# Kernel tuning notes

Hardware: AMD Instinct MI355X
Metric: run time of the kernel (lower is better)

The kernel has to match this reference:

```python
import jax, jax.numpy as jnp
import numpy as np

LN_EPS = 1e-5


def setup_inputs() -> dict:
    key = jax.random.key(0)
    k1, k2, k3, k4, k5 = jax.random.split(key, 5)
    N, D, E, T = 100000, 128, 400000, 4  # nodes, feat dim, edges per etype, n etypes
    feat = jax.random.normal(k1, (N, D), dtype=jnp.float32)
    W = jax.random.normal(k2, (T, D, D), dtype=jnp.float32)
    Wf = jax.random.normal(k3, (T, D, 2 * D), dtype=jnp.float32)
    ln_w = jnp.ones((D,), dtype=jnp.float32)
    ln_b = jnp.zeros((D,), dtype=jnp.float32)
    src = jax.random.randint(k4, (T, E), 0, N, dtype=jnp.int32)
    dst = jax.random.randint(k5, (T, E), 0, N, dtype=jnp.int32)
    return {"feat": feat, "W": W, "Wf": Wf, "ln_w": ln_w, "ln_b": ln_b, "src": src, "dst": dst}


def reference(feat, W, Wf, ln_w, ln_b, src, dst):
    N, D = feat.shape
    T = W.shape[0]
    h = jnp.zeros((N, D), dtype=feat.dtype)
    for t in range(T):  # small fixed loop over edge types (structurally distinct weights)
        msg = feat @ W[t]                    # [N, D] per-src-node projection
        fw = feat @ Wf[t]                    # [N, 2D] FiLM params (dst ntype == src ntype)
        gamma, beta = fw[:, :D], fw[:, D:]
        m = jax.nn.relu(gamma * msg + beta)  # node-wise FiLM + ReLU, pre-scatter
        # copy_u -> gather message at edge src; fn.sum -> segment-sum into dst
        h = h + jax.ops.segment_sum(m[src[t]], dst[t], num_segments=N)
    # LayerNorm (elementwise affine); dropout omitted (eval mode)
    mu = jnp.mean(h, axis=-1, keepdims=True)
    var = jnp.mean(jnp.square(h - mu), axis=-1, keepdims=True)
    out = (h - mu) * jax.lax.rsqrt(var + LN_EPS) * ln_w + ln_b
    return out
```

## Files before the change

### kernel.cpp

```cpp
#include <hip/hip_runtime.h>
#include <hip/hip_bf16.h>

#define DD 128
#define LN_EPS 1e-5f
#define BCAP 3072
#define MAXBIN 1024
#define CHUNK 4096

typedef __bf16 bf16x8 __attribute__((ext_vector_type(8)));
typedef float f32x4 __attribute__((ext_vector_type(4)));

__device__ __forceinline__ float bflo(unsigned int u) { return __uint_as_float(u << 16); }
__device__ __forceinline__ float bfhi(unsigned int u) { return __uint_as_float(u & 0xffff0000u); }

__device__ __forceinline__ void gload_lds16(const void* g, void* lds) {
    __builtin_amdgcn_global_load_lds(
        (const __attribute__((address_space(1))) unsigned int*)g,
        (__attribute__((address_space(3))) unsigned int*)lds, 16, 0, 0);
}

__global__ __launch_bounds__(256) void k_head(const float* __restrict__ feat,
                                              const float* __restrict__ W,
                                              const float* __restrict__ Wf,
                                              const int* __restrict__ dst,
                                              unsigned short* __restrict__ fb,
                                              unsigned short* __restrict__ wcat,
                                              int* __restrict__ H,
                                              int E4, int NBLK, int NBIN, int n8) {
    __shared__ int h[MAXBIN];
    const int b = blockIdx.x, tid = threadIdx.x;

    if (b < NBLK) {
        for (int j = tid; j < NBIN; j += 256) h[j] = 0;
        __syncthreads();
        int base = b * CHUNK;
        int end = base + CHUNK < E4 ? base + CHUNK : E4;
        for (int i = base + tid; i < end; i += 256) atomicAdd(&h[dst[i] >> 7], 1);
        __syncthreads();
        for (int j = tid; j < NBIN; j += 256) H[(size_t)j * NBLK + b] = h[j];
    }

    const int gtid = b * 256 + tid, gsz = gridDim.x * 256;

    for (int i = gtid; i < n8; i += gsz) {
        const float4* p = (const float4*)feat + (size_t)i * 2;
        float4 v0 = p[0], v1 = p[1];
        float vv[8] = {v0.x, v0.y, v0.z, v0.w, v1.x, v1.y, v1.z, v1.w};
        unsigned short u[8];
#pragma unroll
        for (int j = 0; j < 8; j++) {
            __hip_bfloat16 bb = __float2bfloat16(vv[j]);
            u[j] = *reinterpret_cast<unsigned short*>(&bb);
        }
        uint4 o;
        o.x = u[0] | ((unsigned)u[1] << 16);
        o.y = u[2] | ((unsigned)u[3] << 16);
        o.z = u[4] | ((unsigned)u[5] << 16);
        o.w = u[6] | ((unsigned)u[7] << 16);
        ((uint4*)fb)[i] = o;
    }

    for (int i = gtid; i < 4 * 384 * 128; i += gsz) {
        int t = i / (384 * 128);
        int r = i % (384 * 128);
        int c = r / 128, k = r % 128;
        float v = (c < 128) ? W[((size_t)t * 128 + k) * 128 + c]
                            : Wf[((size_t)t * 128 + k) * 256 + (c - 128)];
        __hip_bfloat16 bb = __float2bfloat16(v);
        wcat[i] = *reinterpret_cast<unsigned short*>(&bb);
    }
}

__global__ __launch_bounds__(256) void k_scanbin(int* __restrict__ H, int* __restrict__ C,
                                                 int NBLK, int NBIN) {
    const int wv = (blockIdx.x * 256 + threadIdx.x) >> 6;
    const int lane = threadIdx.x & 63;
    if (wv >= NBIN) return;
    int* row = H + (size_t)wv * NBLK;
    int run = 0;
    for (int base = 0; base < NBLK; base += 64) {
        int idx = base + lane;
        int v = (idx < NBLK) ? row[idx] : 0;
        int s = v;
#pragma unroll
        for (int o = 1; o < 64; o <<= 1) {
            int u = __shfl_up(s, o, 64);
            if (lane >= o) s += u;
        }
        if (idx < NBLK) row[idx] = run + s - v;
        run += __shfl(s, 63, 64);
    }
    if (lane == 0) C[wv] = run;
}

__global__ __launch_bounds__(1024) void k_scan(const int* __restrict__ cnt,
                                               int* __restrict__ off, int NB) {
    __shared__ int s[1024];
    int tid = threadIdx.x;
    s[tid] = (tid < NB) ? cnt[tid] : 0;
    __syncthreads();
    for (int st = 1; st < 1024; st <<= 1) {
        int t = s[tid];
        int a = (tid >= st) ? s[tid - st] : 0;
        __syncthreads();
        s[tid] = t + a;
        __syncthreads();
    }
    if (tid < NB) {
        off[tid] = s[tid] - cnt[tid];
        if (tid == NB - 1) off[NB] = s[tid];
    }
}

__global__ __launch_bounds__(256) void k_place2(const int* __restrict__ src,
                                                const int* __restrict__ dst,
                                                const int* __restrict__ H,
                                                const int* __restrict__ binoff,
                                                unsigned int* __restrict__ rec,
                                                int N, int E, int E4, int NBLK, int NBIN) {
    __shared__ int fill[MAXBIN];
    const int b = blockIdx.x;
    for (int j = threadIdx.x; j < NBIN; j += 256)
        fill[j] = binoff[j] + H[(size_t)j * NBLK + b];
    __syncthreads();
    int base = b * CHUNK;
    int end = base + CHUNK < E4 ? base + CHUNK : E4;
    for (int i = base + threadIdx.x; i < end; i += 256) {
        int d = dst[i];
        int t = i / E;
        unsigned int r = ((unsigned)(d & 127) << 19) | (unsigned)(t * N + src[i]);
        int pos = atomicAdd(&fill[d >> 7], 1);
        rec[pos] = r;
    }
}

__global__ __launch_bounds__(256) void k_sortout(const unsigned int* __restrict__ rec,
                                                 const int* __restrict__ binoff,
                                                 unsigned int* __restrict__ sortedg,
                                                 int* __restrict__ nodestart,
                                                 int* __restrict__ nodedeg, int N) {
    __shared__ int lcnt[128], soff[128], sfill[128], tmp[128];
    __shared__ unsigned int sorted[BCAP];
    const int b = blockIdx.x, tid = threadIdx.x;
    const int s0 = binoff[b];
    int n = binoff[b + 1] - s0;
    if (n > BCAP) n = BCAP;

    if (tid < 128) lcnt[tid] = 0;
    __syncthreads();
    for (int j = tid; j < n; j += 256) atomicAdd(&lcnt[rec[s0 + j] >> 19], 1);
    __syncthreads();
    if (tid < 128) tmp[tid] = lcnt[tid];
    __syncthreads();
    for (int st = 1; st < 128; st <<= 1) {
        int t = 0, a = 0;
        if (tid < 128) {
            t = tmp[tid];
            a = (tid >= st) ? tmp[tid - st] : 0;
        }
        __syncthreads();
        if (tid < 128) tmp[tid] = t + a;
        __syncthreads();
    }
    if (tid < 128) {
        int ex = tmp[tid] - lcnt[tid];
        soff[tid] = ex;
        sfill[tid] = ex;
    }
    __syncthreads();
    for (int j = tid; j < n; j += 256) {
        unsigned int r = rec[s0 + j];
        int p = atomicAdd(&sfill[r >> 19], 1);
        sorted[p] = r & 0x7FFFFu;
    }
    __syncthreads();
    for (int j = tid; j < n; j += 256) sortedg[s0 + j] = sorted[j];
    if (tid < 128) {
        int node = b * 128 + tid;
        if (node < N) {
            nodestart[node] = s0 + soff[tid];
            nodedeg[node] = lcnt[tid];
        }
    }
}

__global__ __launch_bounds__(256, 2) void k_gemm_film(const unsigned short* __restrict__ featb,
                                                      const unsigned short* __restrict__ wcat,
                                                      unsigned short* __restrict__ m, int N,
                                                      int NT) {
    __shared__ unsigned char smem[2 * 16384];
    const int t = blockIdx.y;
    const int tid = threadIdx.x;
    const int w = tid >> 6, lane = tid & 63;
    const int lr = lane & 15, kg = lane >> 4;
    const int cbase = w * 32;

    const unsigned short* wt = wcat + (size_t)t * 384 * 128;
    bf16x8 B[4][3][2];
#pragma unroll
    for (int kkI = 0; kkI < 4; kkI++)
#pragma unroll
        for (int mat = 0; mat < 3; mat++)
#pragma unroll
            for (int cj = 0; cj < 2; cj++) {
                int col = mat * 128 + cbase + cj * 16 + lr;
                B[kkI][mat][cj] = *(const bf16x8*)(wt + (size_t)col * 128 + kkI * 32 + kg * 8);
            }

    auto stage = [&](int buf, int r0) {
#pragma unroll
        for (int it = 0; it < 4; it++) {
            int row = it * 16 + w * 4 + (lane >> 4);
            int gr = r0 + row;
            if (gr >= N) gr = N - 1;
            int x = ((lane & 15) * 16) ^ ((row & 7) << 4);
            const unsigned char* g = (const unsigned char*)featb + (size_t)gr * 256 + x;
            gload_lds16(g, smem + buf * 16384 + it * 4096 + w * 1024);
        }
    };

    unsigned short* mt = m + (size_t)t * N * DD;
    int buf = 0;
    int tile = blockIdx.x;
    if (tile < NT) stage(0, tile * 64);

    for (; tile < NT; tile += gridDim.x) {
        __syncthreads();
        int nxt = tile + gridDim.x;
        if (nxt < NT) stage(buf ^ 1, nxt * 64);

        const unsigned char* sm = smem + buf * 16384;
        f32x4 acc[4][3][2] = {};
#pragma unroll
        for (int kkI = 0; kkI < 4; kkI++) {
            bf16x8 a[4];
#pragma unroll
            for (int mi = 0; mi < 4; mi++) {
                int row = mi * 16 + lr;
                int kb = kkI * 64 + kg * 16;
                a[mi] = *(const bf16x8*)(sm + row * 256 + (kb ^ ((row & 7) << 4)));
            }
#pragma unroll
            for (int mi = 0; mi < 4; mi++)
#pragma unroll
                for (int mat = 0; mat < 3; mat++)
#pragma unroll
                    for (int cj = 0; cj < 2; cj++)
                        acc[mi][mat][cj] = __builtin_amdgcn_mfma_f32_16x16x32_bf16(
                            a[mi], B[kkI][mat][cj], acc[mi][mat][cj], 0, 0, 0);
        }

        const int r0 = tile * 64;
#pragma unroll
        for (int mi = 0; mi < 4; mi++)
#pragma unroll
            for (int cj = 0; cj < 2; cj++)
#pragma unroll
                for (int r = 0; r < 4; r++) {
                    int row = r0 + mi * 16 + kg * 4 + r;
                    if (row < N) {
                        float v = acc[mi][1][cj][r] * acc[mi][0][cj][r] + acc[mi][2][cj][r];
                        v = fmaxf(v, 0.0f);
                        __hip_bfloat16 bb = __float2bfloat16(v);
                        mt[(size_t)row * DD + cbase + cj * 16 + lr] =
                            *reinterpret_cast<unsigned short*>(&bb);
                    }
                }
        buf ^= 1;
    }
}

__global__ __launch_bounds__(256) void k_agg_ln(const unsigned int* __restrict__ sortedg,
                                                const int* __restrict__ nodestart,
                                                const int* __restrict__ nodedeg,
                                                const char* __restrict__ mbase,
                                                const float* __restrict__ lnw,
                                                const float* __restrict__ lnb,
                                                float* __restrict__ out, int N) {
    const int wv = threadIdx.x >> 6, lane = threadIdx.x & 63;
    const int node = blockIdx.x * 4 + wv;
    if (node >= N) return;
    const int start = nodestart[node], deg = nodedeg[node];
    const int q = lane >> 4, sl = lane & 15;
    const unsigned soff = (unsigned)sl * 16u;

    float a[8] = {0.f, 0.f, 0.f, 0.f, 0.f, 0.f, 0.f, 0.f};

    int e = 0;
    for (; e + 16 <= deg; e += 16) {
        unsigned r0 = sortedg[start + e + q];
        unsigned r1 = sortedg[start + e + 4 + q];
        unsigned r2 = sortedg[start + e + 8 + q];
        unsigned r3 = sortedg[start + e + 12 + q];
        uint4 p0 = *(const uint4*)(mbase + (r0 * 256u + soff));
        uint4 p1 = *(const uint4*)(mbase + (r1 * 256u + soff));
        uint4 p2 = *(const uint4*)(mbase + (r2 * 256u + soff));
        uint4 p3 = *(const uint4*)(mbase + (r3 * 256u + soff));
        a[0] += bflo(p0.x) + bflo(p1.x) + bflo(p2.x) + bflo(p3.x);
        a[1] += bfhi(p0.x) + bfhi(p1.x) + bfhi(p2.x) + bfhi(p3.x);
        a[2] += bflo(p0.y) + bflo(p1.y) + bflo(p2.y) + bflo(p3.y);
        a[3] += bfhi(p0.y) + bfhi(p1.y) + bfhi(p2.y) + bfhi(p3.y);
        a[4] += bflo(p0.z) + bflo(p1.z) + bflo(p2.z) + bflo(p3.z);
        a[5] += bfhi(p0.z) + bfhi(p1.z) + bfhi(p2.z) + bfhi(p3.z);
        a[6] += bflo(p0.w) + bflo(p1.w) + bflo(p2.w) + bflo(p3.w);
        a[7] += bfhi(p0.w) + bfhi(p1.w) + bfhi(p2.w) + bfhi(p3.w);
    }
    for (; e + 4 <= deg; e += 4) {
        unsigned r0 = sortedg[start + e + q];
        uint4 p0 = *(const uint4*)(mbase + (r0 * 256u + soff));
        a[0] += bflo(p0.x);
        a[1] += bfhi(p0.x);
        a[2] += bflo(p0.y);
        a[3] += bfhi(p0.y);
        a[4] += bflo(p0.z);
        a[5] += bfhi(p0.z);
        a[6] += bflo(p0.w);
        a[7] += bfhi(p0.w);
    }
    if (e < deg) {
        int idx = e + q;
        float w = (idx < deg) ? 1.0f : 0.0f;
        if (idx >= deg) idx = deg - 1;
        unsigned r0 = sortedg[start + idx];
        uint4 p0 = *(const uint4*)(mbase + (r0 * 256u + soff));
        a[0] += w * bflo(p0.x);
        a[1] += w * bfhi(p0.x);
        a[2] += w * bflo(p0.y);
        a[3] += w * bfhi(p0.y);
        a[4] += w * bflo(p0.z);
        a[5] += w * bfhi(p0.z);
        a[6] += w * bflo(p0.w);
        a[7] += w * bfhi(p0.w);
    }

#pragma unroll
    for (int j = 0; j < 8; j++) {
        a[j] += __shfl_xor(a[j], 16, 64);
        a[j] += __shfl_xor(a[j], 32, 64);
    }
    float s = 0.f, ss = 0.f;
#pragma unroll
    for (int j = 0; j < 8; j++) {
        s += a[j];
        ss += a[j] * a[j];
    }
#pragma unroll
    for (int o = 1; o < 16; o <<= 1) {
        s += __shfl_xor(s, o, 64);
        ss += __shfl_xor(ss, o, 64);
    }
    float mu = s * (1.0f / 128.0f);
    float var = ss * (1.0f / 128.0f) - mu * mu;
    float rstd = rsqrtf(var + LN_EPS);
    if (q == 0) {
        float4 w0 = ((const float4*)lnw)[sl * 2];
        float4 w1 = ((const float4*)lnw)[sl * 2 + 1];
        float4 b0 = ((const float4*)lnb)[sl * 2];
        float4 b1 = ((const float4*)lnb)[sl * 2 + 1];
        float4 o0, o1;
        o0.x = (a[0] - mu) * rstd * w0.x + b0.x;
        o0.y = (a[1] - mu) * rstd * w0.y + b0.y;
        o0.z = (a[2] - mu) * rstd * w0.z + b0.z;
        o0.w = (a[3] - mu) * rstd * w0.w + b0.w;
        o1.x = (a[4] - mu) * rstd * w1.x + b1.x;
        o1.y = (a[5] - mu) * rstd * w1.y + b1.y;
        o1.z = (a[6] - mu) * rstd * w1.z + b1.z;
        o1.w = (a[7] - mu) * rstd * w1.w + b1.w;
        ((float4*)(out + (size_t)node * DD))[sl * 2] = o0;
        ((float4*)(out + (size_t)node * DD))[sl * 2 + 1] = o1;
    }
}

extern "C" void kernel_launch(void* const* d_in, const int* in_sizes, int n_in,
                              void* d_out, int out_size, void* d_ws, size_t ws_size,
                              hipStream_t stream) {
    const float* feat = (const float*)d_in[0];
    const float* W    = (const float*)d_in[1];
    const float* Wf   = (const float*)d_in[2];
    const float* lnw  = (const float*)d_in[3];
    const float* lnb  = (const float*)d_in[4];
    const int* src    = (const int*)d_in[5];
    const int* dst    = (const int*)d_in[6];
    float* out = (float*)d_out;

    const int N = in_sizes[0] / DD;
    const int E = in_sizes[5] / 4;
    const int E4 = 4 * E;
    const int NB = (N + 127) >> 7;
    const int NBLK = (E4 + CHUNK - 1) / CHUNK;
    const int NT = (N + 63) / 64;
    const int n8 = N * DD / 8;

    size_t off = 0;
    char* ws = (char*)d_ws;
    auto alloc = [&](size_t bytes) -> void* {
        void* p = ws + off;
        off += (bytes + 255) & ~(size_t)255;
        return p;
    };
    unsigned short* m     = (unsigned short*)alloc((size_t)4 * N * DD * 2);
    unsigned short* featb = (unsigned short*)alloc((size_t)N * DD * 2);
    unsigned short* wcat  = (unsigned short*)alloc((size_t)4 * 384 * 128 * 2);
    int* H      = (int*)alloc((size_t)NB * NBLK * 4);
    int* C      = (int*)alloc((size_t)NB * 4);
    int* binoff = (int*)alloc((size_t)(NB + 1) * 4);
    unsigned int* rec     = (unsigned int*)alloc((size_t)E4 * 4);
    unsigned int* sortedg = (unsigned int*)alloc((size_t)E4 * 4);
    int* nodestart = (int*)alloc((size_t)N * 4);
    int* nodedeg   = (int*)alloc((size_t)N * 4);
    if (off > ws_size) return;

    k_head<<<2 * NBLK, 256, 0, stream>>>(feat, W, Wf, dst, featb, wcat, H,
                                         E4, NBLK, NB, n8);
    k_scanbin<<<(NB * 64 + 255) / 256, 256, 0, stream>>>(H, C, NBLK, NB);
    k_scan<<<1, 1024, 0, stream>>>(C, binoff, NB);
    k_place2<<<NBLK, 256, 0, stream>>>(src, dst, H, binoff, rec, N, E, E4, NBLK, NB);
    k_sortout<<<NB, 256, 0, stream>>>(rec, binoff, sortedg, nodestart, nodedeg, N);
    dim3 gg(128, 4);
    k_gemm_film<<<gg, 256, 0, stream>>>(featb, wcat, m, N, NT);
    k_agg_ln<<<(N + 3) / 4, 256, 0, stream>>>(sortedg, nodestart, nodedeg,
                                              (const char*)m, lnw, lnb, out, N);
}
```

Measured before the change: 178.0 us.

## Fold bin-offset scan into scanbin via last-block ticket; stage edge indices in LDS

Removes the separate single-block k_scan launch by having the last block of k_scanbin (found with an atomic ticket reset in k_head) compute the global bin offsets. Packs per-node start and degree into one int2 array. In the aggregation kernel, each block cooperatively loads its four nodes' contiguous edge-index range into shared memory before the gather, with a global-memory fallback when it exceeds capacity. This trades a kernel launch and scattered index loads for extra block syncs, a threadfence/atomic handoff, and added shared memory per block.

```diff
diff --git a/kernel.cpp b/kernel.cpp
--- a/kernel.cpp
+++ b/kernel.cpp
@@ -6,6 +6,7 @@
 #define BCAP 3072
 #define MAXBIN 1024
 #define CHUNK 4096
+#define EIDX_CAP 1024
 
 typedef __bf16 bf16x8 __attribute__((ext_vector_type(8)));
 typedef float f32x4 __attribute__((ext_vector_type(4)));
@@ -25,10 +26,11 @@
                                               const int* __restrict__ dst,
                                               unsigned short* __restrict__ fb,
                                               unsigned short* __restrict__ wcat,
-                                              int* __restrict__ H,
+                                              int* __restrict__ H, int* __restrict__ ticket,
                                               int E4, int NBLK, int NBIN, int n8) {
     __shared__ int h[MAXBIN];
     const int b = blockIdx.x, tid = threadIdx.x;
+    if (b == 0 && tid == 0) *ticket = 0;
 
     if (b < NBLK) {
         for (int j = tid; j < NBIN; j += 256) h[j] = 0;
@@ -72,44 +74,68 @@
 }
 
 __global__ __launch_bounds__(256) void k_scanbin(int* __restrict__ H, int* __restrict__ C,
+                                                 int* __restrict__ binoff,
+                                                 int* __restrict__ ticket,
                                                  int NBLK, int NBIN) {
+    __shared__ int s[256];
+    __shared__ int is_last;
     const int wv = (blockIdx.x * 256 + threadIdx.x) >> 6;
     const int lane = threadIdx.x & 63;
-    if (wv >= NBIN) return;
-    int* row = H + (size_t)wv * NBLK;
-    int run = 0;
-    for (int base = 0; base < NBLK; base += 64) {
-        int idx = base + lane;
-        int v = (idx < NBLK) ? row[idx] : 0;
-        int s = v;
-#pragma unroll
-        for (int o = 1; o < 64; o <<= 1) {
-            int u = __shfl_up(s, o, 64);
-            if (lane >= o) s += u;
-        }
-        if (idx < NBLK) row[idx] = run + s - v;
-        run += __shfl(s, 63, 64);
-    }
-    if (lane == 0) C[wv] = run;
-}
-
-__global__ __launch_bounds__(1024) void k_scan(const int* __restrict__ cnt,
-                                               int* __restrict__ off, int NB) {
-    __shared__ int s[1024];
-    int tid = threadIdx.x;
-    s[tid] = (tid < NB) ? cnt[tid] : 0;
-    __syncthreads();
-    for (int st = 1; st < 1024; st <<= 1) {
+    const int tid = threadIdx.x;
+
+    if (wv < NBIN) {
+        int* row = H + (size_t)wv * NBLK;
+        int run = 0;
+        for (int base = 0; base < NBLK; base += 64) {
+            int idx = base + lane;
+            int v = (idx < NBLK) ? row[idx] : 0;
+            int sc = v;
+#pragma unroll
+            for (int o = 1; o < 64; o <<= 1) {
+                int u = __shfl_up(sc, o, 64);
+                if (lane >= o) sc += u;
+            }
+            if (idx < NBLK) row[idx] = run + sc - v;
+            run += __shfl(sc, 63, 64);
+        }
+        if (lane == 0) C[wv] = run;
+    }
+
+    __syncthreads();
+    if (tid == 0) {
+        __threadfence();
+        int v = atomicAdd(ticket, 1);
+        is_last = (v == (int)gridDim.x - 1);
+    }
+    __syncthreads();
+    if (!is_last) return;
+    __threadfence();
+
+    int v[4];
+    int tot = 0;
+#pragma unroll
+    for (int j = 0; j < 4; j++) {
+        int idx = tid * 4 + j;
+        v[j] = (idx < NBIN) ? C[idx] : 0;
+        tot += v[j];
+    }
+    s[tid] = tot;
+    __syncthreads();
+    for (int st = 1; st < 256; st <<= 1) {
         int t = s[tid];
-        int a = (tid >= st) ? s[tid - st] : 0;
-        __syncthreads();
-        s[tid] = t + a;
-        __syncthreads();
-    }
-    if (tid < NB) {
-        off[tid] = s[tid] - cnt[tid];
-        if (tid == NB - 1) off[NB] = s[tid];
-    }
+        int add = (tid >= st) ? s[tid - st] : 0;
+        __syncthreads();
+        s[tid] = t + add;
+        __syncthreads();
+    }
+    int run = s[tid] - tot;
+#pragma unroll
+    for (int j = 0; j < 4; j++) {
+        int idx = tid * 4 + j;
+        if (idx < NBIN) binoff[idx] = run;
+        run += v[j];
+    }
+    if (tid == 255) binoff[NBIN] = s[255];
 }
 
 __global__ __launch_bounds__(256) void k_place2(const int* __restrict__ src,
@@ -137,8 +163,7 @@
 __global__ __launch_bounds__(256) void k_sortout(const unsigned int* __restrict__ rec,
                                                  const int* __restrict__ binoff,
                                                  unsigned int* __restrict__ sortedg,
-                                                 int* __restrict__ nodestart,
-                                                 int* __restrict__ nodedeg, int N) {
+                                                 int2* __restrict__ nodemeta, int N) {
     __shared__ int lcnt[128], soff[128], sfill[128], tmp[128];
     __shared__ unsigned int sorted[BCAP];
     const int b = blockIdx.x, tid = threadIdx.x;
@@ -177,10 +202,7 @@
     for (int j = tid; j < n; j += 256) sortedg[s0 + j] = sorted[j];
     if (tid < 128) {
         int node = b * 128 + tid;
-        if (node < N) {
-            nodestart[node] = s0 + soff[tid];
-            nodedeg[node] = lcnt[tid];
-        }
+        if (node < N) nodemeta[node] = make_int2(s0 + soff[tid], lcnt[tid]);
     }
 }
 
@@ -271,66 +293,114 @@
 }
 
 __global__ __launch_bounds__(256) void k_agg_ln(const unsigned int* __restrict__ sortedg,
-                                                const int* __restrict__ nodestart,
-                                                const int* __restrict__ nodedeg,
+                                                const int2* __restrict__ nodemeta,
                                                 const char* __restrict__ mbase,
                                                 const float* __restrict__ lnw,
                                                 const float* __restrict__ lnb,
                                                 float* __restrict__ out, int N) {
+    __shared__ unsigned eidx[EIDX_CAP];
+    __shared__ int smeta[8];
     const int wv = threadIdx.x >> 6, lane = threadIdx.x & 63;
+    const int tid = threadIdx.x;
     const int node = blockIdx.x * 4 + wv;
+    const int nclamp = node < N ? node : N - 1;
+    const int2 meta = nodemeta[nclamp];
+    if (lane == 0) {
+        smeta[wv * 2] = meta.x;
+        smeta[wv * 2 + 1] = meta.y;
+    }
+    __syncthreads();
+    const int estart0 = smeta[0];
+    const int total = smeta[6] + smeta[7] - estart0;
+    const bool fits = (total <= EIDX_CAP);
+    if (fits)
+        for (int j = tid; j < total; j += 256) eidx[j] = sortedg[estart0 + j];
+    __syncthreads();
     if (node >= N) return;
-    const int start = nodestart[node], deg = nodedeg[node];
+
+    const int deg = meta.y;
     const int q = lane >> 4, sl = lane & 15;
     const unsigned soff = (unsigned)sl * 16u;
-
     float a[8] = {0.f, 0.f, 0.f, 0.f, 0.f, 0.f, 0.f, 0.f};
 
-    int e = 0;
-    for (; e + 16 <= deg; e += 16) {
-        unsigned r0 = sortedg[start + e + q];
-        unsigned r1 = sortedg[start + e + 4 + q];
-        unsigned r2 = sortedg[start + e + 8 + q];
-        unsigned r3 = sortedg[start + e + 12 + q];
-        uint4 p0 = *(const uint4*)(mbase + (r0 * 256u + soff));
-        uint4 p1 = *(const uint4*)(mbase + (r1 * 256u + soff));
-        uint4 p2 = *(const uint4*)(mbase + (r2 * 256u + soff));
-        uint4 p3 = *(const uint4*)(mbase + (r3 * 256u + soff));
-        a[0] += bflo(p0.x) + bflo(p1.x) + bflo(p2.x) + bflo(p3.x);
-        a[1] += bfhi(p0.x) + bfhi(p1.x) + bfhi(p2.x) + bfhi(p3.x);
-        a[2] += bflo(p0.y) + bflo(p1.y) + bflo(p2.y) + bflo(p3.y);
-        a[3] += bfhi(p0.y) + bfhi(p1.y) + bfhi(p2.y) + bfhi(p3.y);
-        a[4] += bflo(p0.z) + bflo(p1.z) + bflo(p2.z) + bflo(p3.z);
-        a[5] += bfhi(p0.z) + bfhi(p1.z) + bfhi(p2.z) + bfhi(p3.z);
-        a[6] += bflo(p0.w) + bflo(p1.w) + bflo(p2.w) + bflo(p3.w);
-        a[7] += bfhi(p0.w) + bfhi(p1.w) + bfhi(p2.w) + bfhi(p3.w);
-    }
-    for (; e + 4 <= deg; e += 4) {
-        unsigned r0 = sortedg[start + e + q];
-        uint4 p0 = *(const uint4*)(mbase + (r0 * 256u + soff));
-        a[0] += bflo(p0.x);
-        a[1] += bfhi(p0.x);
-        a[2] += bflo(p0.y);
-        a[3] += bfhi(p0.y);
-        a[4] += bflo(p0.z);
-        a[5] += bfhi(p0.z);
-        a[6] += bflo(p0.w);
-        a[7] += bfhi(p0.w);
-    }
-    if (e < deg) {
-        int idx = e + q;
-        float w = (idx < deg) ? 1.0f : 0.0f;
-        if (idx >= deg) idx = deg - 1;
-        unsigned r0 = sortedg[start + idx];
-        uint4 p0 = *(const uint4*)(mbase + (r0 * 256u + soff));
-        a[0] += w * bflo(p0.x);
-        a[1] += w * bfhi(p0.x);
-        a[2] += w * bflo(p0.y);
-        a[3] += w * bfhi(p0.y);
-        a[4] += w * bflo(p0.z);
-        a[5] += w * bfhi(p0.z);
-        a[6] += w * bflo(p0.w);
-        a[7] += w * bfhi(p0.w);
+    if (fits) {
+        const int loff = meta.x - estart0;
+        int e = 0;
+        for (; e + 16 <= deg; e += 16) {
+            unsigned r0 = eidx[loff + e + q];
+            unsigned r1 = eidx[loff + e + 4 + q];
+            unsigned r2 = eidx[loff + e + 8 + q];
+            unsigned r3 = eidx[loff + e + 12 + q];
+            uint4 p0 = *(const uint4*)(mbase + (r0 * 256u + soff));
+            uint4 p1 = *(const uint4*)(mbase + (r1 * 256u + soff));
+            uint4 p2 = *(const uint4*)(mbase + (r2 * 256u + soff));
+            uint4 p3 = *(const uint4*)(mbase + (r3 * 256u + soff));
+            a[0] += bflo(p0.x) + bflo(p1.x) + bflo(p2.x) + bflo(p3.x);
+            a[1] += bfhi(p0.x) + bfhi(p1.x) + bfhi(p2.x) + bfhi(p3.x);
+            a[2] += bflo(p0.y) + bflo(p1.y) + bflo(p2.y) + bflo(p3.y);
+            a[3] += bfhi(p0.y) + bfhi(p1.y) + bfhi(p2.y) + bfhi(p3.y);
+            a[4] += bflo(p0.z) + bflo(p1.z) + bflo(p2.z) + bflo(p3.z);
+            a[5] += bfhi(p0.z) + bfhi(p1.z) + bfhi(p2.z) + bfhi(p3.z);
+            a[6] += bflo(p0.w) + bflo(p1.w) + bflo(p2.w) + bflo(p3.w);
+            a[7] += bfhi(p0.w) + bfhi(p1.w) + bfhi(p2.w) + bfhi(p3.w);
+        }
+        for (; e + 4 <= deg; e += 4) {
+            unsigned r0 = eidx[loff + e + q];
+            uint4 p0 = *(const uint4*)(mbase + (r0 * 256u + soff));
+            a[0] += bflo(p0.x);
+            a[1] += bfhi(p0.x);
+            a[2] += bflo(p0.y);
+            a[3] += bfhi(p0.y);
+            a[4] += bflo(p0.z);
+            a[5] += bfhi(p0.z);
+            a[6] += bflo(p0.w);
+            a[7] += bfhi(p0.w);
+        }
+        if (e < deg) {
+            int idx = e + q;
+            float w = (idx < deg) ? 1.0f : 0.0f;
+            if (idx >= deg) idx = deg - 1;
+            unsigned r0 = eidx[loff + idx];
+            uint4 p0 = *(const uint4*)(mbase + (r0 * 256u + soff));
+            a[0] += w * bflo(p0.x);
+            a[1] += w * bfhi(p0.x);
+            a[2] += w * bflo(p0.y);
+            a[3] += w * bfhi(p0.y);
+            a[4] += w * bflo(p0.z);
+            a[5] += w * bfhi(p0.z);
+            a[6] += w * bflo(p0.w);
+            a[7] += w * bfhi(p0.w);
+        }
+    } else {
+        const int start = meta.x;
+        int e = 0;
+        for (; e + 4 <= deg; e += 4) {
+            unsigned r0 = sortedg[start + e + q];
+            uint4 p0 = *(const uint4*)(mbase + (r0 * 256u + soff));
+            a[0] += bflo(p0.x);
+            a[1] += bfhi(p0.x);
+            a[2] += bflo(p0.y);
+            a[3] += bfhi(p0.y);
+            a[4] += bflo(p0.z);
+            a[5] += bfhi(p0.z);
+            a[6] += bflo(p0.w);
+            a[7] += bfhi(p0.w);
+        }
+        if (e < deg) {
+            int idx = e + q;
+            float w = (idx < deg) ? 1.0f : 0.0f;
+            if (idx >= deg) idx = deg - 1;
+            unsigned r0 = sortedg[start + idx];
+            uint4 p0 = *(const uint4*)(mbase + (r0 * 256u + soff));
+            a[0] += w * bflo(p0.x);
+            a[1] += w * bfhi(p0.x);
+            a[2] += w * bflo(p0.y);
+            a[3] += w * bfhi(p0.y);
+            a[4] += w * bflo(p0.z);
+            a[5] += w * bfhi(p0.z);
+            a[6] += w * bflo(p0.w);
+            a[7] += w * bfhi(p0.w);
+        }
     }
 
 #pragma unroll
@@ -404,20 +474,19 @@
     int* H      = (int*)alloc((size_t)NB * NBLK * 4);
     int* C      = (int*)alloc((size_t)NB * 4);
     int* binoff = (int*)alloc((size_t)(NB + 1) * 4);
+    int* ticket = (int*)alloc(256);
     unsigned int* rec     = (unsigned int*)alloc((size_t)E4 * 4);
     unsigned int* sortedg = (unsigned int*)alloc((size_t)E4 * 4);
-    int* nodestart = (int*)alloc((size_t)N * 4);
-    int* nodedeg   = (int*)alloc((size_t)N * 4);
+    int2* nodemeta = (int2*)alloc((size_t)N * 8);
     if (off > ws_size) return;
 
-    k_head<<<2 * NBLK, 256, 0, stream>>>(feat, W, Wf, dst, featb, wcat, H,
+    k_head<<<2 * NBLK, 256, 0, stream>>>(feat, W, Wf, dst, featb, wcat, H, ticket,
                                          E4, NBLK, NB, n8);
-    k_scanbin<<<(NB * 64 + 255) / 256, 256, 0, stream>>>(H, C, NBLK, NB);
-    k_scan<<<1, 1024, 0, stream>>>(C, binoff, NB);
+    k_scanbin<<<(NB * 64 + 255) / 256, 256, 0, stream>>>(H, C, binoff, ticket, NBLK, NB);
     k_place2<<<NBLK, 256, 0, stream>>>(src, dst, H, binoff, rec, N, E, E4, NBLK, NB);
-    k_sortout<<<NB, 256, 0, stream>>>(rec, binoff, sortedg, nodestart, nodedeg, N);
+    k_sortout<<<NB, 256, 0, stream>>>(rec, binoff, sortedg, nodemeta, N);
     dim3 gg(128, 4);
     k_gemm_film<<<gg, 256, 0, stream>>>(featb, wcat, m, N, NT);
-    k_agg_ln<<<(N + 3) / 4, 256, 0, stream>>>(sortedg, nodestart, nodedeg,
+    k_agg_ln<<<(N + 3) / 4, 256, 0, stream>>>(sortedg, nodemeta,
                                               (const char*)m, lnw, lnb, out, N);
 }
```

Result: faster. 169.5 us (-4.7%).
